# Kernel optimization log

Hardware: AMD Instinct MI355X
Metric: run time of the kernel (lower is better)

## Reference

```python
import jax, jax.numpy as jnp
import numpy as np

D_IN = 256
D_OUT = 256
NUM_HEADS = 8
D_INNER = D_OUT * NUM_HEADS  # 2048
D_HID = int(D_OUT * 4.0)     # 1024
B, H, W = 16, 56, 56
N = 1 + H * W                # 3137 (CLS + spatial)
LN_EPS = 1e-5
L2_EPS = 1e-12


def layer_norm(x, g, b):
    mu = jnp.mean(x, axis=-1, keepdims=True)
    var = jnp.mean(jnp.square(x - mu), axis=-1, keepdims=True)
    return (x - mu) * jax.lax.rsqrt(var + LN_EPS) * g + b


def l2_normalize(x, axis):
    n = jnp.sqrt(jnp.sum(x * x, axis=axis, keepdims=True))
    return x / jnp.maximum(n, L2_EPS)


def setup_inputs() -> dict:
    key = jax.random.key(0)
    ks = jax.random.split(key, 16)
    s = 0.02
    return {
        "x": jax.random.normal(ks[0], (B, N, D_IN), dtype=jnp.float32),
        "norm1_w": jnp.ones((D_IN,), jnp.float32),
        "norm1_b": jnp.zeros((D_IN,), jnp.float32),
        "wq": jax.random.normal(ks[1], (D_INNER, D_IN), jnp.float32) * s,
        "bq": jnp.zeros((D_INNER,), jnp.float32),
        "wk": jax.random.normal(ks[2], (D_INNER, D_IN), jnp.float32) * s,
        "bk": jnp.zeros((D_INNER,), jnp.float32),
        "w_g": jax.random.normal(ks[3], (D_INNER, 1), jnp.float32),
        "wp": jax.random.normal(ks[4], (D_INNER, D_INNER), jnp.float32) * s,
        "bp": jnp.zeros((D_INNER,), jnp.float32),
        "wf": jax.random.normal(ks[5], (D_OUT, D_INNER), jnp.float32) * s,
        "bf": jnp.zeros((D_OUT,), jnp.float32),
        "norm2_w": jnp.ones((D_OUT,), jnp.float32),
        "norm2_b": jnp.zeros((D_OUT,), jnp.float32),
        "w1": jax.random.normal(ks[6], (D_HID, D_OUT), jnp.float32) * s,
        "b1": jnp.zeros((D_HID,), jnp.float32),
        "w2": jax.random.normal(ks[7], (D_OUT, D_HID), jnp.float32) * s,
        "b2": jnp.zeros((D_OUT,), jnp.float32),
        "h": H,
        "w": W,
    }


def reference(x, norm1_w, norm1_b, wq, bq, wk, bk, w_g, wp, bp, wf, bf,
              norm2_w, norm2_b, w1, b1, w2, b2, h, w):
    scale = D_OUT ** (-0.5)
    # --- attention branch ---
    xn = layer_norm(x, norm1_w, norm1_b)                 # [B,N,D]
    q = xn @ wq.T + bq                                   # [B,N,Di]
    k = xn @ wk.T + bk                                   # [B,N,Di]
    q = l2_normalize(q, axis=-1)
    k = l2_normalize(k, axis=-1)
    A = (q @ w_g) * scale                                # [B,N,1]
    A = l2_normalize(A, axis=1)                          # normalize over tokens
    G = jnp.sum(A * q, axis=1)                           # [B,Di]
    out = (G[:, None, :] * k) @ wp.T + bp + q            # [B,N,Di]
    attn = out @ wf.T + bf                               # [B,N,Do]
    x = x + attn
    # --- pointwise-conv MLP branch (1x1 convs == per-token linears) ---
    xn2 = layer_norm(x, norm2_w, norm2_b)
    cls_tok = xn2[:, :1]                                 # CLS bypasses the MLP
    body = xn2[:, 1:]                                    # [B,h*w,Do]
    hdn = jax.nn.gelu(body @ w1.T + b1, approximate=False)
    body = hdn @ w2.T + b2
    mlp_out = jnp.concatenate([cls_tok, body], axis=1)
    return x + mlp_out
```

## Files before the change

kernel.cpp:

```cpp
#include <hip/hip_runtime.h>
#include <hip/hip_bf16.h>
#include <stdint.h>

typedef __bf16 bf16x8 __attribute__((ext_vector_type(8)));
typedef float f32x4 __attribute__((ext_vector_type(4)));
typedef unsigned short ushort_t;

static constexpr int kB = 16;
static constexpr int kN = 3137;
static constexpr long kM = (long)kB * kN;
static constexpr int kNS = 64;

__device__ __forceinline__ float bf2f(ushort_t u) {
  return __uint_as_float(((unsigned)u) << 16);
}
__device__ __forceinline__ ushort_t f2bf(float f) {
  __hip_bfloat16 h = __float2bfloat16(f);
  return *reinterpret_cast<ushort_t*>(&h);
}
__device__ __forceinline__ void gload16(const void* g, void* l) {
  __builtin_amdgcn_global_load_lds(
      (const __attribute__((address_space(1))) unsigned int*)g,
      (__attribute__((address_space(3))) unsigned int*)(uintptr_t)l,
      16, 0, 0);
}
__device__ __forceinline__ f32x4 mfma16(bf16x8 a, bf16x8 b, f32x4 c) {
  return __builtin_amdgcn_mfma_f32_16x16x32_bf16(a, b, c, 0, 0, 0);
}


__global__ __launch_bounds__(256) void cast_kernel(const float* __restrict__ s,
                                                   ushort_t* __restrict__ d, long n4) {
  long i = (long)blockIdx.x * 256 + threadIdx.x;
  if (i >= n4) return;
  float4 v = *(const float4*)(s + i * 4);
  ushort4 o;
  o.x = f2bf(v.x); o.y = f2bf(v.y); o.z = f2bf(v.z); o.w = f2bf(v.w);
  *(ushort4*)(d + i * 4) = o;
}

__global__ __launch_bounds__(256) void transpose_cast_kernel(const float* __restrict__ src,
                                                             ushort_t* __restrict__ dst,
                                                             int R, int C) {
  __shared__ float tile[32][33];
  const int tx = blockIdx.x * 32, ty = blockIdx.y * 32;
  const int x = threadIdx.x & 31, y0 = threadIdx.x >> 5;
#pragma unroll
  for (int j = 0; j < 32; j += 8)
    tile[y0 + j][x] = src[(long)(ty + y0 + j) * C + tx + x];
  __syncthreads();
#pragma unroll
  for (int j = 0; j < 32; j += 8)
    dst[(long)(tx + y0 + j) * R + ty + x] = f2bf(tile[x][y0 + j]);
}

__global__ __launch_bounds__(256) void gemv_kernel(const ushort_t* __restrict__ A,
                                                   const float* __restrict__ v,
                                                   const float* __restrict__ add,
                                                   float* __restrict__ out, int rows,
                                                   int K) {
  int row = blockIdx.x * 4 + (threadIdx.x >> 6);
  if (row >= rows) return;
  int lane = threadIdx.x & 63;
  float acc = 0.f;
  for (int k0 = lane * 8; k0 < K; k0 += 512) {
    uint4 raw = *(const uint4*)(A + (long)row * K + k0);
    const ushort_t* u = (const ushort_t*)&raw;
#pragma unroll
    for (int j = 0; j < 8; ++j) acc += bf2f(u[j]) * v[k0 + j];
  }
#pragma unroll
  for (int o = 32; o >= 1; o >>= 1) acc += __shfl_xor(acc, o);
  if (lane == 0) out[row] = (add ? add[row] : 0.f) + acc;
}

__global__ __launch_bounds__(256) void scalars_kernel(const float* __restrict__ bq,
                                                      const float* __restrict__ bk,
                                                      const float* __restrict__ wg,
                                                      float* __restrict__ scal) {
  __shared__ float red[3][4];
  float s0 = 0, s1 = 0, s2 = 0;
  for (int i = threadIdx.x; i < 2048; i += 256) {
    s0 += bq[i] * bq[i];
    s1 += bk[i] * bk[i];
    s2 += bq[i] * wg[i];
  }
#pragma unroll
  for (int o = 32; o >= 1; o >>= 1) {
    s0 += __shfl_xor(s0, o); s1 += __shfl_xor(s1, o); s2 += __shfl_xor(s2, o);
  }
  int w = threadIdx.x >> 6;
  if ((threadIdx.x & 63) == 0) { red[0][w] = s0; red[1][w] = s1; red[2][w] = s2; }
  __syncthreads();
  if (threadIdx.x < 3)
    scal[threadIdx.x] = red[threadIdx.x][0] + red[threadIdx.x][1] +
                        red[threadIdx.x][2] + red[threadIdx.x][3];
}

__global__ __launch_bounds__(256) void ln_kernel(
    const float* __restrict__ x, const float* __restrict__ gw,
    const float* __restrict__ gb, ushort_t* __restrict__ out, long M,
    const float* __restrict__ uqv, const float* __restrict__ ukv,
    const float* __restrict__ vgv, float* __restrict__ duq,
    float* __restrict__ duk, float* __restrict__ dvg) {
  long row = (long)blockIdx.x * 4 + (threadIdx.x >> 6);
  if (row >= M) return;
  int lane = threadIdx.x & 63;
  float4 v = *(const float4*)(x + row * 256 + lane * 4);
  float s = v.x + v.y + v.z + v.w;
  float s2 = v.x * v.x + v.y * v.y + v.z * v.z + v.w * v.w;
#pragma unroll
  for (int o = 32; o >= 1; o >>= 1) {
    s += __shfl_xor(s, o);
    s2 += __shfl_xor(s2, o);
  }
  float mu = s * (1.f / 256.f);
  float var = fmaxf(s2 * (1.f / 256.f) - mu * mu, 0.f);
  float rsd = rsqrtf(var + 1e-5f);
  float e[4];
  ushort4 o4;
  e[0] = bf2f(o4.x = f2bf((v.x - mu) * rsd * gw[lane * 4 + 0] + gb[lane * 4 + 0]));
  e[1] = bf2f(o4.y = f2bf((v.y - mu) * rsd * gw[lane * 4 + 1] + gb[lane * 4 + 1]));
  e[2] = bf2f(o4.z = f2bf((v.z - mu) * rsd * gw[lane * 4 + 2] + gb[lane * 4 + 2]));
  e[3] = bf2f(o4.w = f2bf((v.w - mu) * rsd * gw[lane * 4 + 3] + gb[lane * 4 + 3]));
  *(ushort4*)(out + row * 256 + lane * 4) = o4;
  if (duq) {
    int base = lane * 4;
    float a = e[0] * uqv[base] + e[1] * uqv[base + 1] + e[2] * uqv[base + 2] + e[3] * uqv[base + 3];
    float b = e[0] * ukv[base] + e[1] * ukv[base + 1] + e[2] * ukv[base + 2] + e[3] * ukv[base + 3];
    float c = e[0] * vgv[base] + e[1] * vgv[base + 1] + e[2] * vgv[base + 2] + e[3] * vgv[base + 3];
#pragma unroll
    for (int o = 32; o >= 1; o >>= 1) {
      a += __shfl_xor(a, o); b += __shfl_xor(b, o); c += __shfl_xor(c, o);
    }
    if (lane == 0) { duq[row] = a; duk[row] = b; dvg[row] = c; }
  }
}

__global__ __launch_bounds__(256) void reduce_rows_kernel(
    const float* __restrict__ part, const float* __restrict__ duq,
    const float* __restrict__ duk, const float* __restrict__ dvg,
    const float* __restrict__ scal, float* __restrict__ rs_q,
    float* __restrict__ rs_k, float* __restrict__ Av) {
  long i = (long)blockIdx.x * 256 + threadIdx.x;
  if (i >= kM) return;
  float sq = 0.f, sk = 0.f;
#pragma unroll
  for (int s = 0; s < 8; ++s) sq += part[(long)s * kM + i];
#pragma unroll
  for (int s = 8; s < 16; ++s) sk += part[(long)s * kM + i];
  sq += 2.f * duq[i] + scal[0];
  sk += 2.f * duk[i] + scal[1];
  float rq = 1.f / fmaxf(sqrtf(fmaxf(sq, 0.f)), 1e-12f);
  float rk = 1.f / fmaxf(sqrtf(fmaxf(sk, 0.f)), 1e-12f);
  rs_q[i] = rq;
  rs_k[i] = rk;
  Av[i] = rq * (dvg[i] + scal[2]) * 0.0625f;
}

__global__ __launch_bounds__(256) void anorm_kernel(const float* __restrict__ Av,
                                                    float* __restrict__ invA) {
  int b = blockIdx.x;
  __shared__ float red[4];
  float s = 0.f;
  for (int n = threadIdx.x; n < kN; n += 256) {
    float a = Av[(long)b * kN + n];
    s += a * a;
  }
#pragma unroll
  for (int o = 32; o >= 1; o >>= 1) s += __shfl_xor(s, o);
  if ((threadIdx.x & 63) == 0) red[threadIdx.x >> 6] = s;
  __syncthreads();
  if (threadIdx.x == 0)
    invA[b] = 1.f / fmaxf(sqrtf(red[0] + red[1] + red[2] + red[3]), 1e-12f);
}

__global__ __launch_bounds__(256) void tvec_kernel(const ushort_t* __restrict__ xn,
                                                   const float* __restrict__ Av,
                                                   const float* __restrict__ rs_q,
                                                   const float* __restrict__ invA,
                                                   float* __restrict__ tpart,
                                                   float* __restrict__ Spart) {
  const int ns = blockIdx.x, b = blockIdx.y;
  const int n0 = ns * 50;
  int cnt = kN - n0; if (cnt > 50) cnt = 50; if (cnt < 0) cnt = 0;
  __shared__ float c_lds[50];
  const int t = threadIdx.x;
  if (t < cnt) {
    long gi = (long)b * kN + n0 + t;
    c_lds[t] = invA[b] * Av[gi] * rs_q[gi];
  }
  __syncthreads();
  float acc = 0.f;
  const ushort_t* p = xn + ((long)b * kN + n0) * 256 + t;
  for (int i = 0; i < cnt; ++i, p += 256) acc += c_lds[i] * bf2f(*p);
  tpart[((long)ns * 16 + b) * 256 + t] = acc;
  if (t == 0) {
    float s = 0.f;
    for (int i = 0; i < cnt; ++i) s += c_lds[i];
    Spart[ns * 16 + b] = s;
  }
}

__global__ __launch_bounds__(256) void treduce_kernel(const float* __restrict__ tpart,
                                                      const float* __restrict__ Spart,
                                                      float* __restrict__ tb,
                                                      float* __restrict__ S) {
  int b = blockIdx.x, e = threadIdx.x;
  float s = 0.f;
  for (int ns = 0; ns < kNS; ++ns) s += tpart[((long)ns * 16 + b) * 256 + e];
  tb[b * 256 + e] = s;
  if (e == 0) {
    float ss = 0.f;
    for (int ns = 0; ns < kNS; ++ns) ss += Spart[ns * 16 + b];
    S[b] = ss;
  }
}

__global__ __launch_bounds__(256) void gvec_kernel(const float* __restrict__ wq,
                                                   const float* __restrict__ bq,
                                                   const float* __restrict__ tb,
                                                   const float* __restrict__ S,
                                                   float* __restrict__ G) {
  int i = blockIdx.x * 4 + (threadIdx.x >> 6);
  int b = i >> 11, d = i & 2047;
  int lane = threadIdx.x & 63;
  float4 w4 = *(const float4*)(wq + (long)d * 256 + lane * 4);
  const float* tv = tb + b * 256 + lane * 4;
  float acc = w4.x * tv[0] + w4.y * tv[1] + w4.z * tv[2] + w4.w * tv[3];
#pragma unroll
  for (int o = 32; o >= 1; o >>= 1) acc += __shfl_xor(acc, o);
  if (lane == 0) G[i] = acc + bq[d] * S[b];
}

__global__ __launch_bounds__(256) void wfpg_kernel(const ushort_t* __restrict__ wfp,
                                                   const float* __restrict__ G,
                                                   ushort_t* __restrict__ wfpG) {
  long i = ((long)blockIdx.x * 256 + threadIdx.x) * 8;
  int b = (int)(i >> 19);
  long rem = i & 524287;
  int d = (int)(rem & 2047);
  uint4 raw = *(const uint4*)(wfp + rem);
  ushort_t* u = (ushort_t*)&raw;
  const float* g = G + b * 2048 + d;
#pragma unroll
  for (int j = 0; j < 8; ++j) u[j] = f2bf(bf2f(u[j]) * g[j]);
  *(uint4*)(wfpG + (long)b * 524288 + rem) = raw;
}

template <int EPI, int LDO>
__global__ __launch_bounds__(512) void gemm_kernel(
    const ushort_t* __restrict__ A, const ushort_t* __restrict__ W,
    const ushort_t* __restrict__ W2, int M, int K, int NT, int MT,
    const float* __restrict__ b1, const float* __restrict__ b2,
    const float* __restrict__ b3, const float* __restrict__ rs1,
    const float* __restrict__ rs2, const float* __restrict__ auxf,
    const ushort_t* __restrict__ auxb, void* __restrict__ out0,
    float* __restrict__ partbuf, long zA, long zW2, long zRow, int zB2) {
  constexpr bool DUAL = (EPI == 9);
  constexpr int BUFB = DUAL ? 24576 : 16384;
  __shared__ char smem[2 * BUFB];

  const int t = threadIdx.x;
  const int wid = t >> 6, lane = t & 63;
  const int frow = lane & 15, kg = lane >> 4;
  const int wm = (wid >> 2) * 64;
  const int wn = (wid & 3) * 32;

  const int total = (int)gridDim.x;
  const int qq = total >> 3, rr = total & 7;
  const int xb = blockIdx.x & 7, ib = blockIdx.x >> 3;
  const int lg = (xb < rr ? xb * (qq + 1) : rr * (qq + 1) + (xb - rr) * qq) + ib;
  const int nt = lg % NT;
  const int mt = (lg / NT) % MT;
  const int z = lg / (NT * MT);
  const int n0 = nt * 128, m0 = mt * 128;

  A += (long)z * zA;
  const ushort_t* W2z = nullptr;
  if constexpr (DUAL) W2z = W2 + (long)z * zW2;

  const int srow = t >> 2;
  const int csw = ((t & 3) ^ ((t >> 3) & 3)) * 8;
  long arow = m0 + srow; if (arow > M - 1) arow = M - 1;
  const ushort_t* gA = A + arow * K + csw;
  const ushort_t* gW = W + (long)(n0 + srow) * K + csw;
  const ushort_t* gW2 = nullptr;
  if constexpr (DUAL) gW2 = W2z + (long)(n0 + srow) * K + csw;

  f32x4 acc[4][2];
  f32x4 accd[4][2];
#pragma unroll
  for (int mi = 0; mi < 4; ++mi)
#pragma unroll
    for (int ni = 0; ni < 2; ++ni) {
      acc[mi][ni] = f32x4{0.f, 0.f, 0.f, 0.f};
      if constexpr (DUAL) accd[mi][ni] = f32x4{0.f, 0.f, 0.f, 0.f};
    }

  const int KT = K >> 5;
  auto stage = [&](int bi, int k0) {
    char* base = smem + bi * BUFB + (wid << 10);
    gload16(gA + k0, base);
    gload16(gW + k0, base + 8192);
    if constexpr (DUAL) gload16(gW2 + k0, base + 16384);
  };

  stage(0, 0);
  __syncthreads();
  for (int kt = 0; kt < KT; ++kt) {
    const int cur = kt & 1;
    if (kt + 1 < KT) stage(cur ^ 1, (kt + 1) << 5);
    const char* bA = smem + cur * BUFB;
    bf16x8 af[4], bw[2], bw2[2];
#pragma unroll
    for (int mi = 0; mi < 4; ++mi) {
      int r = wm + mi * 16 + frow;
      af[mi] = *(const bf16x8*)(bA + r * 64 + ((kg ^ ((r >> 1) & 3)) << 4));
    }
#pragma unroll
    for (int ni = 0; ni < 2; ++ni) {
      int r = wn + ni * 16 + frow;
      int sw = (kg ^ ((r >> 1) & 3)) << 4;
      bw[ni] = *(const bf16x8*)(bA + 8192 + r * 64 + sw);
      if constexpr (DUAL) bw2[ni] = *(const bf16x8*)(bA + 16384 + r * 64 + sw);
    }
#pragma unroll
    for (int mi = 0; mi < 4; ++mi)
#pragma unroll
      for (int ni = 0; ni < 2; ++ni) {
        acc[mi][ni] = mfma16(af[mi], bw[ni], acc[mi][ni]);
        if constexpr (DUAL) accd[mi][ni] = mfma16(af[mi], bw2[ni], accd[mi][ni]);
      }
    __syncthreads();
  }

  if constexpr (EPI == 10) {
#pragma unroll
    for (int mi = 0; mi < 4; ++mi)
#pragma unroll
      for (int j = 0; j < 4; ++j) {
        const int gmi = m0 + wm + mi * 16 + kg * 4 + j;
        float rp = 0.f;
        if (gmi < M) {
#pragma unroll
          for (int ni = 0; ni < 2; ++ni) {
            const int gn = n0 + wn + ni * 16 + frow;
            rp += acc[mi][ni][j] * bf2f(A[(long)gmi * K + (gn & 255)]);
          }
        }
#pragma unroll
        for (int off = 1; off <= 8; off <<= 1) rp += __shfl_xor(rp, off);
        if (frow == 0 && gmi < M)
          partbuf[(long)(nt * 4 + (wid & 3)) * M + gmi] = rp;
      }
    return;
  }

  if constexpr (EPI == 3 || EPI == 5) {
#pragma unroll
    for (int mi = 0; mi < 4; ++mi)
#pragma unroll
      for (int ni = 0; ni < 2; ++ni) {
        const int gn = n0 + wn + ni * 16 + frow;
        const int lcolb = (wn + ni * 16 + frow) * 2;
#pragma unroll
        for (int j = 0; j < 4; ++j) {
          const int lrow = wm + mi * 16 + kg * 4 + j;
          float v = acc[mi][ni][j];
          if (b1) v += b1[gn];
          if constexpr (EPI == 3)
            v = 0.5f * v * (1.0f + erff(v * 0.70710678118654752f));
          *(ushort_t*)(smem + lrow * 256 + (lcolb ^ ((lrow & 7) << 4))) = f2bf(v);
        }
      }
    __syncthreads();
#pragma unroll
    for (int p = 0; p < 4; ++p) {
      const int r = p * 32 + (t >> 4);
      const int cb = (t & 15) * 16;
      uint4 v = *(const uint4*)(smem + r * 256 + (cb ^ ((r & 7) << 4)));
      const int gmi = m0 + r;
      if (gmi < M)
        *(uint4*)((ushort_t*)out0 + ((long)z * zRow + gmi) * LDO + n0 + cb / 2) = v;
    }
    return;
  }

#pragma unroll
  for (int mi = 0; mi < 4; ++mi)
#pragma unroll
    for (int ni = 0; ni < 2; ++ni) {
      const int gn = n0 + wn + ni * 16 + frow;
#pragma unroll
      for (int j = 0; j < 4; ++j) {
        const int gmi = m0 + wm + mi * 16 + kg * 4 + j;
        if (gmi >= M) continue;
        const long grow = (long)z * zRow + gmi;
        const long idx = grow * LDO + gn;
        if constexpr (EPI == 4) {
          float v = acc[mi][ni][j] + b1[gn];
          const bool cls = (gmi % kN) == 0;
          ((float*)out0)[idx] += cls ? bf2f(auxb[idx]) : v;
        } else {
          float v = auxf[idx] + rs1[grow] * (acc[mi][ni][j] + b1[gn]) + b3[gn] +
                    rs2[grow] * (accd[mi][ni][j] + b2[z * zB2 + gn]);
          ((float*)out0)[idx] = v;
        }
      }
    }
}


extern "C" void kernel_launch(void* const* d_in, const int* in_sizes, int n_in,
                              void* d_out, int out_size, void* d_ws, size_t ws_size,
                              hipStream_t stream) {
  const float* x = (const float*)d_in[0];
  const float* n1w = (const float*)d_in[1];
  const float* n1b = (const float*)d_in[2];
  const float* wq = (const float*)d_in[3];
  const float* bq = (const float*)d_in[4];
  const float* wk = (const float*)d_in[5];
  const float* bk = (const float*)d_in[6];
  const float* wg = (const float*)d_in[7];
  const float* wp = (const float*)d_in[8];
  const float* bp = (const float*)d_in[9];
  const float* wf = (const float*)d_in[10];
  const float* bfv = (const float*)d_in[11];
  const float* n2w = (const float*)d_in[12];
  const float* n2b = (const float*)d_in[13];
  const float* w1 = (const float*)d_in[14];
  const float* b1 = (const float*)d_in[15];
  const float* w2 = (const float*)d_in[16];
  const float* b2 = (const float*)d_in[17];
  float* out = (float*)d_out;

  char* ws = (char*)d_ws;
  size_t off = 0;
  auto alloc = [&](size_t bytes) {
    size_t o = off;
    off += (bytes + 255) & ~(size_t)255;
    return o;
  };
  ushort_t* wqT = (ushort_t*)(ws + alloc((size_t)256 * 2048 * 2));
  ushort_t* wkT = (ushort_t*)(ws + alloc((size_t)256 * 2048 * 2));
  ushort_t* wpT = (ushort_t*)(ws + alloc((size_t)2048 * 2048 * 2));
  ushort_t* wf_bf = (ushort_t*)(ws + alloc((size_t)256 * 2048 * 2));
  ushort_t* w1_bf = (ushort_t*)(ws + alloc((size_t)1024 * 256 * 2));
  ushort_t* w2_bf = (ushort_t*)(ws + alloc((size_t)256 * 1024 * 2));
  ushort_t* MqMk = (ushort_t*)(ws + alloc((size_t)512 * 256 * 2));
  ushort_t* wfq_bf = (ushort_t*)(ws + alloc((size_t)256 * 256 * 2));
  ushort_t* wfp_bf = (ushort_t*)(ws + alloc((size_t)256 * 2048 * 2));
  ushort_t* wfpG = (ushort_t*)(ws + alloc((size_t)16 * 256 * 2048 * 2));
  ushort_t* Wc = (ushort_t*)(ws + alloc((size_t)16 * 256 * 256 * 2));
  float* uq = (float*)(ws + alloc(256 * 4));
  float* uk = (float*)(ws + alloc(256 * 4));
  float* vg = (float*)(ws + alloc(256 * 4));
  float* cfq = (float*)(ws + alloc(256 * 4));
  float* cvec = (float*)(ws + alloc(256 * 4));
  float* cb = (float*)(ws + alloc((size_t)16 * 256 * 4));
  float* scal = (float*)(ws + alloc(256));
  ushort_t* xn = (ushort_t*)(ws + alloc((size_t)kM * 256 * 2));
  float* duq = (float*)(ws + alloc((size_t)kM * 4));
  float* duk = (float*)(ws + alloc((size_t)kM * 4));
  float* dvg = (float*)(ws + alloc((size_t)kM * 4));
  float* part = (float*)(ws + alloc((size_t)16 * kM * 4));
  float* rs_q = (float*)(ws + alloc((size_t)kM * 4));
  float* rs_k = (float*)(ws + alloc((size_t)kM * 4));
  float* Av = (float*)(ws + alloc((size_t)kM * 4));
  float* invA = (float*)(ws + alloc(64));
  float* tpart = (float*)(ws + alloc((size_t)kNS * 16 * 256 * 4));
  float* Spart = (float*)(ws + alloc((size_t)kNS * 16 * 4));
  float* tb = (float*)(ws + alloc((size_t)16 * 256 * 4));
  float* Sb = (float*)(ws + alloc(64));
  float* G = (float*)(ws + alloc((size_t)16 * 2048 * 4));
  ushort_t* hdn = (ushort_t*)(ws + alloc((size_t)kM * 1024 * 2));
  if (off > ws_size) return;

  transpose_cast_kernel<<<dim3(8, 64), 256, 0, stream>>>(wq, wqT, 2048, 256);
  transpose_cast_kernel<<<dim3(8, 64), 256, 0, stream>>>(wk, wkT, 2048, 256);
  transpose_cast_kernel<<<dim3(64, 64), 256, 0, stream>>>(wp, wpT, 2048, 2048);
  cast_kernel<<<512, 256, 0, stream>>>(wf, wf_bf, 256 * 2048 / 4);
  cast_kernel<<<256, 256, 0, stream>>>(w1, w1_bf, 1024 * 256 / 4);
  cast_kernel<<<256, 256, 0, stream>>>(w2, w2_bf, 256 * 1024 / 4);
  gemv_kernel<<<64, 256, 0, stream>>>(wqT, bq, nullptr, uq, 256, 2048);
  gemv_kernel<<<64, 256, 0, stream>>>(wkT, bk, nullptr, uk, 256, 2048);
  gemv_kernel<<<64, 256, 0, stream>>>(wqT, wg, nullptr, vg, 256, 2048);
  gemv_kernel<<<64, 256, 0, stream>>>(wf_bf, bq, nullptr, cfq, 256, 2048);
  gemv_kernel<<<64, 256, 0, stream>>>(wf_bf, bp, bfv, cvec, 256, 2048);
  scalars_kernel<<<1, 256, 0, stream>>>(bq, bk, wg, scal);
  gemm_kernel<5, 256><<<4, 512, 0, stream>>>(
      wqT, wqT, nullptr, 256, 2048, 2, 2, nullptr, nullptr, nullptr, nullptr,
      nullptr, nullptr, nullptr, MqMk, nullptr, 0, 0, 0, 0);
  gemm_kernel<5, 256><<<4, 512, 0, stream>>>(
      wkT, wkT, nullptr, 256, 2048, 2, 2, nullptr, nullptr, nullptr, nullptr,
      nullptr, nullptr, nullptr, MqMk + 65536, nullptr, 0, 0, 0, 0);
  gemm_kernel<5, 256><<<4, 512, 0, stream>>>(
      wf_bf, wqT, nullptr, 256, 2048, 2, 2, nullptr, nullptr, nullptr, nullptr,
      nullptr, nullptr, nullptr, wfq_bf, nullptr, 0, 0, 0, 0);
  gemm_kernel<5, 2048><<<32, 512, 0, stream>>>(
      wf_bf, wpT, nullptr, 256, 2048, 16, 2, nullptr, nullptr, nullptr, nullptr,
      nullptr, nullptr, nullptr, wfp_bf, nullptr, 0, 0, 0, 0);

  ln_kernel<<<(int)((kM + 3) / 4), 256, 0, stream>>>(x, n1w, n1b, xn, kM, uq, uk, vg,
                                                     duq, duk, dvg);
  gemm_kernel<10, 256><<<1572, 512, 0, stream>>>(
      xn, MqMk, nullptr, (int)kM, 256, 4, 393, nullptr, nullptr, nullptr, nullptr,
      nullptr, nullptr, nullptr, nullptr, part, 0, 0, 0, 0);
  reduce_rows_kernel<<<(int)((kM + 255) / 256), 256, 0, stream>>>(
      part, duq, duk, dvg, scal, rs_q, rs_k, Av);
  anorm_kernel<<<16, 256, 0, stream>>>(Av, invA);

  tvec_kernel<<<dim3(kNS, 16), 256, 0, stream>>>(xn, Av, rs_q, invA, tpart, Spart);
  treduce_kernel<<<16, 256, 0, stream>>>(tpart, Spart, tb, Sb);
  gvec_kernel<<<16 * 2048 / 4, 256, 0, stream>>>(wq, bq, tb, Sb, G);

  wfpg_kernel<<<4096, 256, 0, stream>>>(wfp_bf, G, wfpG);
  gemv_kernel<<<1024, 256, 0, stream>>>(wfpG, bk, nullptr, cb, 16 * 256, 2048);
  gemm_kernel<5, 256><<<64, 512, 0, stream>>>(
      wfpG, wkT, nullptr, 256, 2048, 2, 2, nullptr, nullptr, nullptr, nullptr,
      nullptr, nullptr, nullptr, Wc, nullptr, 524288, 0, 256, 0);

  gemm_kernel<9, 256><<<800, 512, 0, stream>>>(
      xn, wfq_bf, Wc, kN, 256, 2, 25, cfq, cb, cvec, rs_q, rs_k, x, nullptr, out,
      nullptr, (long)kN * 256, 65536, kN, 256);

  ln_kernel<<<(int)((kM + 3) / 4), 256, 0, stream>>>(out, n2w, n2b, xn, kM, nullptr,
                                                     nullptr, nullptr, nullptr,
                                                     nullptr, nullptr);
  gemm_kernel<3, 1024><<<3144, 512, 0, stream>>>(
      xn, w1_bf, nullptr, (int)kM, 256, 8, 393, b1, nullptr, nullptr, nullptr,
      nullptr, nullptr, nullptr, hdn, nullptr, 0, 0, 0, 0);
  gemm_kernel<4, 256><<<786, 512, 0, stream>>>(
      hdn, w2_bf, nullptr, (int)kM, 1024, 2, 393, b2, nullptr, nullptr, nullptr,
      nullptr, nullptr, xn, out, nullptr, 0, 0, 0, 0);
}
```

Measured before the change: 455.6 us.

## Fuse attention output with LayerNorm2 and fuse MLP up/GELU/down into one kernel

Replaces the dual-weight attention-output GEMM and the second LayerNorm with one kernel. It computes full 256-wide rows, writes the residual, then normalises in-block to produce xn2. The two MLP GEMMs are merged into a single kernel that keeps the 1024-wide hidden activation in LDS in 128-column chunks, so the bf16 hidden buffer never goes through global memory. It also swaps exact erf GELU for a tanh-style approximation via exp2, which adds numerical error. The fused kernels use large dynamic LDS (80KB and 144KB), so occupancy drops to one block per CU.

```diff
diff --git a/kernel.cpp b/kernel.cpp
--- a/kernel.cpp
+++ b/kernel.cpp
@@ -26,6 +26,11 @@
 }
 __device__ __forceinline__ f32x4 mfma16(bf16x8 a, bf16x8 b, f32x4 c) {
   return __builtin_amdgcn_mfma_f32_16x16x32_bf16(a, b, c, 0, 0, 0);
+}
+__device__ __forceinline__ float gelu_fast(float v) {
+  float u = v * (0.79788456f + 0.03567740814f * v * v);
+  float e = exp2f(u * 2.8853900817779268f);
+  return v - v * (1.0f / (1.0f + e));
 }
 
 
@@ -250,23 +255,15 @@
 
 template <int EPI, int LDO>
 __global__ __launch_bounds__(512) void gemm_kernel(
-    const ushort_t* __restrict__ A, const ushort_t* __restrict__ W,
-    const ushort_t* __restrict__ W2, int M, int K, int NT, int MT,
-    const float* __restrict__ b1, const float* __restrict__ b2,
-    const float* __restrict__ b3, const float* __restrict__ rs1,
-    const float* __restrict__ rs2, const float* __restrict__ auxf,
-    const ushort_t* __restrict__ auxb, void* __restrict__ out0,
-    float* __restrict__ partbuf, long zA, long zW2, long zRow, int zB2) {
-  constexpr bool DUAL = (EPI == 9);
-  constexpr int BUFB = DUAL ? 24576 : 16384;
-  __shared__ char smem[2 * BUFB];
-
+    const ushort_t* __restrict__ A, const ushort_t* __restrict__ W, int M, int K,
+    int NT, int MT, const float* __restrict__ b1, void* __restrict__ out0,
+    float* __restrict__ partbuf, long zA, long zRow) {
+  __shared__ char smem[2 * 16384];
   const int t = threadIdx.x;
   const int wid = t >> 6, lane = t & 63;
   const int frow = lane & 15, kg = lane >> 4;
   const int wm = (wid >> 2) * 64;
   const int wn = (wid & 3) * 32;
-
   const int total = (int)gridDim.x;
   const int qq = total >> 3, rr = total & 7;
   const int xb = blockIdx.x & 7, ib = blockIdx.x >> 3;
@@ -275,44 +272,33 @@
   const int mt = (lg / NT) % MT;
   const int z = lg / (NT * MT);
   const int n0 = nt * 128, m0 = mt * 128;
-
   A += (long)z * zA;
-  const ushort_t* W2z = nullptr;
-  if constexpr (DUAL) W2z = W2 + (long)z * zW2;
 
   const int srow = t >> 2;
   const int csw = ((t & 3) ^ ((t >> 3) & 3)) * 8;
   long arow = m0 + srow; if (arow > M - 1) arow = M - 1;
   const ushort_t* gA = A + arow * K + csw;
   const ushort_t* gW = W + (long)(n0 + srow) * K + csw;
-  const ushort_t* gW2 = nullptr;
-  if constexpr (DUAL) gW2 = W2z + (long)(n0 + srow) * K + csw;
 
   f32x4 acc[4][2];
-  f32x4 accd[4][2];
 #pragma unroll
   for (int mi = 0; mi < 4; ++mi)
 #pragma unroll
-    for (int ni = 0; ni < 2; ++ni) {
-      acc[mi][ni] = f32x4{0.f, 0.f, 0.f, 0.f};
-      if constexpr (DUAL) accd[mi][ni] = f32x4{0.f, 0.f, 0.f, 0.f};
-    }
+    for (int ni = 0; ni < 2; ++ni) acc[mi][ni] = f32x4{0.f, 0.f, 0.f, 0.f};
 
   const int KT = K >> 5;
   auto stage = [&](int bi, int k0) {
-    char* base = smem + bi * BUFB + (wid << 10);
+    char* base = smem + bi * 16384 + (wid << 10);
     gload16(gA + k0, base);
     gload16(gW + k0, base + 8192);
-    if constexpr (DUAL) gload16(gW2 + k0, base + 16384);
   };
-
   stage(0, 0);
   __syncthreads();
   for (int kt = 0; kt < KT; ++kt) {
     const int cur = kt & 1;
     if (kt + 1 < KT) stage(cur ^ 1, (kt + 1) << 5);
-    const char* bA = smem + cur * BUFB;
-    bf16x8 af[4], bw[2], bw2[2];
+    const char* bA = smem + cur * 16384;
+    bf16x8 af[4], bw[2];
 #pragma unroll
     for (int mi = 0; mi < 4; ++mi) {
       int r = wm + mi * 16 + frow;
@@ -321,17 +307,12 @@
 #pragma unroll
     for (int ni = 0; ni < 2; ++ni) {
       int r = wn + ni * 16 + frow;
-      int sw = (kg ^ ((r >> 1) & 3)) << 4;
-      bw[ni] = *(const bf16x8*)(bA + 8192 + r * 64 + sw);
-      if constexpr (DUAL) bw2[ni] = *(const bf16x8*)(bA + 16384 + r * 64 + sw);
+      bw[ni] = *(const bf16x8*)(bA + 8192 + r * 64 + ((kg ^ ((r >> 1) & 3)) << 4));
     }
 #pragma unroll
     for (int mi = 0; mi < 4; ++mi)
 #pragma unroll
-      for (int ni = 0; ni < 2; ++ni) {
-        acc[mi][ni] = mfma16(af[mi], bw[ni], acc[mi][ni]);
-        if constexpr (DUAL) accd[mi][ni] = mfma16(af[mi], bw2[ni], accd[mi][ni]);
-      }
+      for (int ni = 0; ni < 2; ++ni) acc[mi][ni] = mfma16(af[mi], bw[ni], acc[mi][ni]);
     __syncthreads();
   }
 
@@ -357,56 +338,298 @@
     return;
   }
 
-  if constexpr (EPI == 3 || EPI == 5) {
-#pragma unroll
-    for (int mi = 0; mi < 4; ++mi)
-#pragma unroll
-      for (int ni = 0; ni < 2; ++ni) {
-        const int gn = n0 + wn + ni * 16 + frow;
-        const int lcolb = (wn + ni * 16 + frow) * 2;
-#pragma unroll
-        for (int j = 0; j < 4; ++j) {
-          const int lrow = wm + mi * 16 + kg * 4 + j;
-          float v = acc[mi][ni][j];
-          if (b1) v += b1[gn];
-          if constexpr (EPI == 3)
-            v = 0.5f * v * (1.0f + erff(v * 0.70710678118654752f));
-          *(ushort_t*)(smem + lrow * 256 + (lcolb ^ ((lrow & 7) << 4))) = f2bf(v);
-        }
-      }
-    __syncthreads();
-#pragma unroll
-    for (int p = 0; p < 4; ++p) {
-      const int r = p * 32 + (t >> 4);
-      const int cb = (t & 15) * 16;
-      uint4 v = *(const uint4*)(smem + r * 256 + (cb ^ ((r & 7) << 4)));
-      const int gmi = m0 + r;
-      if (gmi < M)
-        *(uint4*)((ushort_t*)out0 + ((long)z * zRow + gmi) * LDO + n0 + cb / 2) = v;
-    }
-    return;
-  }
-
 #pragma unroll
   for (int mi = 0; mi < 4; ++mi)
 #pragma unroll
     for (int ni = 0; ni < 2; ++ni) {
       const int gn = n0 + wn + ni * 16 + frow;
+      const int lcolb = (wn + ni * 16 + frow) * 2;
 #pragma unroll
       for (int j = 0; j < 4; ++j) {
-        const int gmi = m0 + wm + mi * 16 + kg * 4 + j;
-        if (gmi >= M) continue;
-        const long grow = (long)z * zRow + gmi;
-        const long idx = grow * LDO + gn;
-        if constexpr (EPI == 4) {
-          float v = acc[mi][ni][j] + b1[gn];
-          const bool cls = (gmi % kN) == 0;
-          ((float*)out0)[idx] += cls ? bf2f(auxb[idx]) : v;
+        const int lrow = wm + mi * 16 + kg * 4 + j;
+        float v = acc[mi][ni][j];
+        if (b1) v += b1[gn];
+        *(ushort_t*)(smem + lrow * 256 + (lcolb ^ ((lrow & 7) << 4))) = f2bf(v);
+      }
+    }
+  __syncthreads();
+#pragma unroll
+  for (int p = 0; p < 4; ++p) {
+    const int r = p * 32 + (t >> 4);
+    const int cb = (t & 15) * 16;
+    uint4 v = *(const uint4*)(smem + r * 256 + (cb ^ ((r & 7) << 4)));
+    const int gmi = m0 + r;
+    if (gmi < M)
+      *(uint4*)((ushort_t*)out0 + ((long)z * zRow + gmi) * LDO + n0 + cb / 2) = v;
+  }
+}
+
+__global__ __launch_bounds__(512) void dualln_kernel(
+    const ushort_t* __restrict__ xn, const ushort_t* __restrict__ Wq,
+    const ushort_t* __restrict__ Wc, const float* __restrict__ cfq,
+    const float* __restrict__ cb, const float* __restrict__ cvec,
+    const float* __restrict__ rs1, const float* __restrict__ rs2,
+    const float* __restrict__ xres, const float* __restrict__ n2w,
+    const float* __restrict__ n2b, float* __restrict__ out,
+    ushort_t* __restrict__ xn2) {
+  constexpr int BUFB = 40960;
+  extern __shared__ char smem[];
+  const int t = threadIdx.x, wid = t >> 6, lane = t & 63;
+  const int frow = lane & 15, kg = lane >> 4;
+  const int wm = (wid >> 2) * 64, wn = (wid & 3) * 64;
+  const int total = (int)gridDim.x;
+  const int qq = total >> 3, rr = total & 7;
+  const int xb = blockIdx.x & 7, ib = blockIdx.x >> 3;
+  const int lg = (xb < rr ? xb * (qq + 1) : rr * (qq + 1) + (xb - rr) * qq) + ib;
+  const int mt = lg % 25, z = lg / 25;
+  const int m0 = mt * 128;
+  const ushort_t* A = xn + (long)z * kN * 256;
+  const ushort_t* W2z = Wc + (long)z * 65536;
+  const int csw = ((t & 3) ^ ((t >> 3) & 3)) * 8;
+  int arow = m0 + (t >> 2); if (arow > kN - 1) arow = kN - 1;
+  const ushort_t* gA = A + (long)arow * 256 + csw;
+  const ushort_t* gW0 = Wq + (long)(t >> 2) * 256 + csw;
+  const ushort_t* gW1 = Wq + (long)(128 + (t >> 2)) * 256 + csw;
+  const ushort_t* gV0 = W2z + (long)(t >> 2) * 256 + csw;
+  const ushort_t* gV1 = W2z + (long)(128 + (t >> 2)) * 256 + csw;
+
+  f32x4 acc[4][4], accd[4][4];
+#pragma unroll
+  for (int mi = 0; mi < 4; ++mi)
+#pragma unroll
+    for (int ni = 0; ni < 4; ++ni) {
+      acc[mi][ni] = f32x4{0.f, 0.f, 0.f, 0.f};
+      accd[mi][ni] = f32x4{0.f, 0.f, 0.f, 0.f};
+    }
+
+  auto stage = [&](int bi, int k0) {
+    char* b = smem + bi * BUFB + (wid << 10);
+    gload16(gA + k0, b);
+    gload16(gW0 + k0, b + 8192);
+    gload16(gW1 + k0, b + 16384);
+    gload16(gV0 + k0, b + 24576);
+    gload16(gV1 + k0, b + 32768);
+  };
+  stage(0, 0);
+  __syncthreads();
+  for (int kt = 0; kt < 8; ++kt) {
+    if (kt < 7) stage((kt + 1) & 1, (kt + 1) * 32);
+    const char* bb = smem + (kt & 1) * BUFB;
+    bf16x8 af[4], bw[4], bv[4];
+#pragma unroll
+    for (int mi = 0; mi < 4; ++mi) {
+      int r = wm + mi * 16 + frow;
+      af[mi] = *(const bf16x8*)(bb + r * 64 + ((kg ^ ((r >> 1) & 3)) << 4));
+    }
+#pragma unroll
+    for (int ni = 0; ni < 4; ++ni) {
+      int r = wn + ni * 16 + frow;
+      int sw = (kg ^ ((r >> 1) & 3)) << 4;
+      bw[ni] = *(const bf16x8*)(bb + 8192 + r * 64 + sw);
+      bv[ni] = *(const bf16x8*)(bb + 24576 + r * 64 + sw);
+    }
+#pragma unroll
+    for (int mi = 0; mi < 4; ++mi)
+#pragma unroll
+      for (int ni = 0; ni < 4; ++ni) {
+        acc[mi][ni] = mfma16(af[mi], bw[ni], acc[mi][ni]);
+        accd[mi][ni] = mfma16(af[mi], bv[ni], accd[mi][ni]);
+      }
+    __syncthreads();
+  }
+
+  float* red_s = (float*)smem;
+  float* red_q = (float*)(smem + 2048);
+  float* mu_l = (float*)(smem + 4096);
+  float* rl_l = (float*)(smem + 4608);
+#pragma unroll
+  for (int mi = 0; mi < 4; ++mi)
+#pragma unroll
+    for (int j = 0; j < 4; ++j) {
+      const int row = wm + mi * 16 + kg * 4 + j;
+      const int gmi = m0 + row;
+      const bool valid = gmi < kN;
+      const long grow = (long)z * kN + (valid ? gmi : kN - 1);
+      const float r1 = rs1[grow], r2 = rs2[grow];
+      float s = 0.f, q = 0.f;
+#pragma unroll
+      for (int ni = 0; ni < 4; ++ni) {
+        const int gn = wn + ni * 16 + frow;
+        const long idx = grow * 256 + gn;
+        float v = xres[idx] + r1 * (acc[mi][ni][j] + cfq[gn]) + cvec[gn] +
+                  r2 * (accd[mi][ni][j] + cb[z * 256 + gn]);
+        if (valid) out[idx] = v;
+        acc[mi][ni][j] = v;
+        s += v;
+        q += v * v;
+      }
+#pragma unroll
+      for (int off = 1; off <= 8; off <<= 1) {
+        s += __shfl_xor(s, off);
+        q += __shfl_xor(q, off);
+      }
+      if (frow == 0) {
+        red_s[(wid & 3) * 128 + row] = s;
+        red_q[(wid & 3) * 128 + row] = q;
+      }
+    }
+  __syncthreads();
+  if (t < 128) {
+    float s = red_s[t] + red_s[128 + t] + red_s[256 + t] + red_s[384 + t];
+    float q = red_q[t] + red_q[128 + t] + red_q[256 + t] + red_q[384 + t];
+    float mu = s * (1.f / 256.f);
+    float var = fmaxf(q * (1.f / 256.f) - mu * mu, 0.f);
+    mu_l[t] = mu;
+    rl_l[t] = rsqrtf(var + 1e-5f);
+  }
+  __syncthreads();
+#pragma unroll
+  for (int mi = 0; mi < 4; ++mi)
+#pragma unroll
+    for (int j = 0; j < 4; ++j) {
+      const int row = wm + mi * 16 + kg * 4 + j;
+      const int gmi = m0 + row;
+      if (gmi >= kN) continue;
+      const long grow = (long)z * kN + gmi;
+      const float mu = mu_l[row], rl = rl_l[row];
+#pragma unroll
+      for (int ni = 0; ni < 4; ++ni) {
+        const int gn = wn + ni * 16 + frow;
+        xn2[grow * 256 + gn] =
+            f2bf((acc[mi][ni][j] - mu) * rl * n2w[gn] + n2b[gn]);
+      }
+    }
+}
+
+__global__ __launch_bounds__(512) void mlp_kernel(
+    const ushort_t* __restrict__ xn2, const ushort_t* __restrict__ w1g,
+    const float* __restrict__ b1v, const ushort_t* __restrict__ w2g,
+    const float* __restrict__ b2v, float* __restrict__ out) {
+  extern __shared__ char smem[];
+  const int t = threadIdx.x, wid = t >> 6, lane = t & 63;
+  const int frow = lane & 15, kg = lane >> 4;
+  const int wm = (wid >> 2) * 64;
+  const int wn1 = (wid & 3) * 32;
+  const int wn2 = (wid & 3) * 64;
+  const long m0 = (long)blockIdx.x * 128;
+  int V = (int)(kM - m0); if (V > 128) V = 128;
+
+#pragma unroll
+  for (int p = 0; p < 8; ++p) {
+    int c = p * 512 + t;
+    int row = c >> 5, ch = c & 31;
+    long gr = m0 + (row < V ? row : V - 1);
+    gload16(xn2 + gr * 256 + ((ch ^ (row & 7)) * 8), smem + p * 8192 + (wid << 10));
+  }
+  const int csw = ((t & 3) ^ ((t >> 3) & 3)) * 8;
+  auto stage_w1 = [&](int h, int kt, int bi) {
+    gload16(w1g + ((long)(h * 128 + (t >> 2))) * 256 + kt * 32 + csw,
+            smem + 98304 + bi * 8192 + (wid << 10));
+  };
+  auto stage_w2 = [&](int h, int kt2, int bi) {
+    gload16(w2g + ((long)(t >> 2)) * 1024 + h * 128 + kt2 * 32 + csw,
+            smem + 114688 + bi * 16384 + (wid << 10));
+    gload16(w2g + ((long)(128 + (t >> 2))) * 1024 + h * 128 + kt2 * 32 + csw,
+            smem + 114688 + bi * 16384 + 8192 + (wid << 10));
+  };
+
+  f32x4 acc2[4][4];
+#pragma unroll
+  for (int mi = 0; mi < 4; ++mi)
+#pragma unroll
+    for (int ni = 0; ni < 4; ++ni) acc2[mi][ni] = f32x4{0.f, 0.f, 0.f, 0.f};
+
+  stage_w1(0, 0, 0);
+  __syncthreads();
+
+  for (int h = 0; h < 8; ++h) {
+    f32x4 acc1[4][2];
+#pragma unroll
+    for (int mi = 0; mi < 4; ++mi)
+#pragma unroll
+      for (int ni = 0; ni < 2; ++ni) acc1[mi][ni] = f32x4{0.f, 0.f, 0.f, 0.f};
+    for (int kt = 0; kt < 8; ++kt) {
+      if (kt < 7) stage_w1(h, kt + 1, (kt + 1) & 1);
+      else stage_w2(h, 0, 0);
+      const char* wb = smem + 98304 + (kt & 1) * 8192;
+      bf16x8 af[4], bw[2];
+#pragma unroll
+      for (int mi = 0; mi < 4; ++mi) {
+        int r = wm + mi * 16 + frow;
+        af[mi] = *(const bf16x8*)(smem + r * 512 + (((kt * 4 + kg) ^ (r & 7)) << 4));
+      }
+#pragma unroll
+      for (int ni = 0; ni < 2; ++ni) {
+        int r = wn1 + ni * 16 + frow;
+        bw[ni] = *(const bf16x8*)(wb + r * 64 + ((kg ^ ((r >> 1) & 3)) << 4));
+      }
+#pragma unroll
+      for (int mi = 0; mi < 4; ++mi)
+#pragma unroll
+        for (int ni = 0; ni < 2; ++ni) acc1[mi][ni] = mfma16(af[mi], bw[ni], acc1[mi][ni]);
+      __syncthreads();
+    }
+    float bb[2];
+#pragma unroll
+    for (int ni = 0; ni < 2; ++ni) bb[ni] = b1v[h * 128 + wn1 + ni * 16 + frow];
+#pragma unroll
+    for (int mi = 0; mi < 4; ++mi)
+#pragma unroll
+      for (int ni = 0; ni < 2; ++ni)
+#pragma unroll
+        for (int j = 0; j < 4; ++j) {
+          const int row = wm + mi * 16 + kg * 4 + j;
+          const int col = wn1 + ni * 16 + frow;
+          float g = gelu_fast(acc1[mi][ni][j] + bb[ni]);
+          *(ushort_t*)(smem + 65536 + row * 256 + (((col >> 3) ^ (row & 7)) << 4) +
+                       (col & 7) * 2) = f2bf(g);
+        }
+    __syncthreads();
+    for (int kt2 = 0; kt2 < 4; ++kt2) {
+      if (kt2 < 3) stage_w2(h, kt2 + 1, (kt2 + 1) & 1);
+      else if (h < 7) stage_w1(h + 1, 0, 0);
+      const char* wb2 = smem + 114688 + (kt2 & 1) * 16384;
+      bf16x8 af[4], bw[4];
+#pragma unroll
+      for (int mi = 0; mi < 4; ++mi) {
+        int r = wm + mi * 16 + frow;
+        af[mi] = *(const bf16x8*)(smem + 65536 + r * 256 +
+                                  (((kt2 * 4 + kg) ^ (r & 7)) << 4));
+      }
+#pragma unroll
+      for (int ni = 0; ni < 4; ++ni) {
+        int r = wn2 + ni * 16 + frow;
+        bw[ni] = *(const bf16x8*)(wb2 + r * 64 + ((kg ^ ((r >> 1) & 3)) << 4));
+      }
+#pragma unroll
+      for (int mi = 0; mi < 4; ++mi)
+#pragma unroll
+        for (int ni = 0; ni < 4; ++ni) acc2[mi][ni] = mfma16(af[mi], bw[ni], acc2[mi][ni]);
+      __syncthreads();
+    }
+  }
+
+#pragma unroll
+  for (int mi = 0; mi < 4; ++mi)
+#pragma unroll
+    for (int j = 0; j < 4; ++j) {
+      const int row = wm + mi * 16 + kg * 4 + j;
+      if (row >= V) continue;
+      const long gmi = m0 + row;
+      const bool cls = (gmi % kN) == 0;
+#pragma unroll
+      for (int ni = 0; ni < 4; ++ni) {
+        const int col = wn2 + ni * 16 + frow;
+        const long idx = gmi * 256 + col;
+        float add;
+        if (cls) {
+          ushort_t u = *(const ushort_t*)(smem + row * 512 +
+                                          (((col >> 3) ^ (row & 7)) << 4) + (col & 7) * 2);
+          add = bf2f(u);
         } else {
-          float v = auxf[idx] + rs1[grow] * (acc[mi][ni][j] + b1[gn]) + b3[gn] +
-                    rs2[grow] * (accd[mi][ni][j] + b2[z * zB2 + gn]);
-          ((float*)out0)[idx] = v;
+          add = acc2[mi][ni][j] + b2v[col];
         }
+        out[idx] += add;
       }
     }
 }
@@ -474,7 +697,6 @@
   float* tb = (float*)(ws + alloc((size_t)16 * 256 * 4));
   float* Sb = (float*)(ws + alloc(64));
   float* G = (float*)(ws + alloc((size_t)16 * 2048 * 4));
-  ushort_t* hdn = (ushort_t*)(ws + alloc((size_t)kM * 1024 * 2));
   if (off > ws_size) return;
 
   transpose_cast_kernel<<<dim3(8, 64), 256, 0, stream>>>(wq, wqT, 2048, 256);
@@ -489,24 +711,19 @@
   gemv_kernel<<<64, 256, 0, stream>>>(wf_bf, bq, nullptr, cfq, 256, 2048);
   gemv_kernel<<<64, 256, 0, stream>>>(wf_bf, bp, bfv, cvec, 256, 2048);
   scalars_kernel<<<1, 256, 0, stream>>>(bq, bk, wg, scal);
-  gemm_kernel<5, 256><<<4, 512, 0, stream>>>(
-      wqT, wqT, nullptr, 256, 2048, 2, 2, nullptr, nullptr, nullptr, nullptr,
-      nullptr, nullptr, nullptr, MqMk, nullptr, 0, 0, 0, 0);
-  gemm_kernel<5, 256><<<4, 512, 0, stream>>>(
-      wkT, wkT, nullptr, 256, 2048, 2, 2, nullptr, nullptr, nullptr, nullptr,
-      nullptr, nullptr, nullptr, MqMk + 65536, nullptr, 0, 0, 0, 0);
-  gemm_kernel<5, 256><<<4, 512, 0, stream>>>(
-      wf_bf, wqT, nullptr, 256, 2048, 2, 2, nullptr, nullptr, nullptr, nullptr,
-      nullptr, nullptr, nullptr, wfq_bf, nullptr, 0, 0, 0, 0);
-  gemm_kernel<5, 2048><<<32, 512, 0, stream>>>(
-      wf_bf, wpT, nullptr, 256, 2048, 16, 2, nullptr, nullptr, nullptr, nullptr,
-      nullptr, nullptr, nullptr, wfp_bf, nullptr, 0, 0, 0, 0);
+  gemm_kernel<5, 256><<<4, 512, 0, stream>>>(wqT, wqT, 256, 2048, 2, 2, nullptr,
+                                             MqMk, nullptr, 0, 0);
+  gemm_kernel<5, 256><<<4, 512, 0, stream>>>(wkT, wkT, 256, 2048, 2, 2, nullptr,
+                                             MqMk + 65536, nullptr, 0, 0);
+  gemm_kernel<5, 256><<<4, 512, 0, stream>>>(wf_bf, wqT, 256, 2048, 2, 2, nullptr,
+                                             wfq_bf, nullptr, 0, 0);
+  gemm_kernel<5, 2048><<<32, 512, 0, stream>>>(wf_bf, wpT, 256, 2048, 16, 2, nullptr,
+                                               wfp_bf, nullptr, 0, 0);
 
   ln_kernel<<<(int)((kM + 3) / 4), 256, 0, stream>>>(x, n1w, n1b, xn, kM, uq, uk, vg,
                                                      duq, duk, dvg);
-  gemm_kernel<10, 256><<<1572, 512, 0, stream>>>(
-      xn, MqMk, nullptr, (int)kM, 256, 4, 393, nullptr, nullptr, nullptr, nullptr,
-      nullptr, nullptr, nullptr, nullptr, part, 0, 0, 0, 0);
+  gemm_kernel<10, 256><<<1572, 512, 0, stream>>>(xn, MqMk, (int)kM, 256, 4, 393,
+                                                 nullptr, nullptr, part, 0, 0);
   reduce_rows_kernel<<<(int)((kM + 255) / 256), 256, 0, stream>>>(
       part, duq, duk, dvg, scal, rs_q, rs_k, Av);
   anorm_kernel<<<16, 256, 0, stream>>>(Av, invA);
@@ -517,21 +734,11 @@
 
   wfpg_kernel<<<4096, 256, 0, stream>>>(wfp_bf, G, wfpG);
   gemv_kernel<<<1024, 256, 0, stream>>>(wfpG, bk, nullptr, cb, 16 * 256, 2048);
-  gemm_kernel<5, 256><<<64, 512, 0, stream>>>(
-      wfpG, wkT, nullptr, 256, 2048, 2, 2, nullptr, nullptr, nullptr, nullptr,
-      nullptr, nullptr, nullptr, Wc, nullptr, 524288, 0, 256, 0);
-
-  gemm_kernel<9, 256><<<800, 512, 0, stream>>>(
-      xn, wfq_bf, Wc, kN, 256, 2, 25, cfq, cb, cvec, rs_q, rs_k, x, nullptr, out,
-      nullptr, (long)kN * 256, 65536, kN, 256);
-
-  ln_kernel<<<(int)((kM + 3) / 4), 256, 0, stream>>>(out, n2w, n2b, xn, kM, nullptr,
-                                                     nullptr, nullptr, nullptr,
-                                                     nullptr, nullptr);
-  gemm_kernel<3, 1024><<<3144, 512, 0, stream>>>(
-      xn, w1_bf, nullptr, (int)kM, 256, 8, 393, b1, nullptr, nullptr, nullptr,
-      nullptr, nullptr, nullptr, hdn, nullptr, 0, 0, 0, 0);
-  gemm_kernel<4, 256><<<786, 512, 0, stream>>>(
-      hdn, w2_bf, nullptr, (int)kM, 1024, 2, 393, b2, nullptr, nullptr, nullptr,
-      nullptr, nullptr, xn, out, nullptr, 0, 0, 0, 0);
-}
+  gemm_kernel<5, 256><<<64, 512, 0, stream>>>(wfpG, wkT, 256, 2048, 2, 2, nullptr,
+                                              Wc, nullptr, 524288, 256);
+
+  dualln_kernel<<<400, 512, 81920, stream>>>(xn, wfq_bf, Wc, cfq, cb, cvec, rs_q,
+                                             rs_k, x, n2w, n2b, out, xn);
+
+  mlp_kernel<<<393, 512, 147456, stream>>>(xn, w1_bf, b1, w2_bf, b2, out);
+}
```

After: 507.4 us. +11.4%, slower.
